# Kernel optimization log

Measured on AMD Instinct MI355X. Metric: run time of the kernel, lower is better.

The kernel has to match this reference:

```python
import jax, jax.numpy as jnp
import numpy as np

T, D, E, I = 2048, 2048, 16, 1408  # tokens, hidden, experts, moe intermediate


def setup_inputs() -> dict:
    key = jax.random.key(0)
    k1, k2, k3, k4 = jax.random.split(key, 4)
    return {
        "hidden_states": jax.random.normal(k1, (T, D), dtype=jnp.float32),
        "gate_w": jax.random.normal(k2, (E, D), dtype=jnp.float32) * 0.02,
        "w13": jax.random.normal(k3, (E, 2 * I, D), dtype=jnp.float32) * 0.02,
        "w2": jax.random.normal(k4, (E, D, I), dtype=jnp.float32) * 0.02,
        "top_k": 6,
    }


def reference(hidden_states, gate_w, w13, w2, top_k):
    x = hidden_states                               # [T, D]
    n_tokens, n_experts = x.shape[0], gate_w.shape[0]

    # Router gate + softmax + top-k (select_experts, use_grouped_topk=False)
    router_logits = x @ gate_w.T                    # [T, E]
    probs = jax.nn.softmax(router_logits, axis=-1)
    topk_w, topk_ids = jax.lax.top_k(probs, top_k)  # [T, K]
    # renormalize=True
    topk_w = topk_w / jnp.sum(topk_w, axis=-1, keepdims=True)

    # Dense combine weights [T, E]: scatter top-k weights to their experts
    combine = jnp.zeros((n_tokens, n_experts), dtype=x.dtype)
    combine = combine.at[jnp.arange(n_tokens)[:, None], topk_ids].add(topk_w)

    # Fused MoE experts: SwiGLU (w13 = fused gate+up), activation='silu'
    w1g = w13[:, : w13.shape[1] // 2, :]            # [E, I, D] gate proj
    w1u = w13[:, w13.shape[1] // 2 :, :]            # [E, I, D] up proj
    g = jnp.einsum("td,eid->tei", x, w1g)           # [T, E, I]
    u = jnp.einsum("td,eid->tei", x, w1u)
    h = jax.nn.silu(g) * u                          # [T, E, I]
    # Down proj + weighted combine over experts
    out = jnp.einsum("tei,edi,te->td", h, w2, combine)  # [T, D]
    return out
```

## Files before the change

### kernel.cpp

```cpp
#include <hip/hip_runtime.h>

#define T_TOK 2048
#define DIM 2048
#define NE 16
#define NI 1408
#define TOPK 6

typedef __bf16 bf16x8 __attribute__((ext_vector_type(8)));
typedef float f32x4 __attribute__((ext_vector_type(4)));

static __device__ __forceinline__ unsigned short f2bf(float f) {
  unsigned int u = __builtin_bit_cast(unsigned int, f);
  u += 0x7fffu + ((u >> 16) & 1u);
  return (unsigned short)(u >> 16);
}

static __device__ __forceinline__ void async_load16(const void* g, void* l) {
  __builtin_amdgcn_global_load_lds(
      (const __attribute__((address_space(1))) unsigned int*)g,
      (__attribute__((address_space(3))) unsigned int*)l, 16, 0, 0);
}

__global__ __launch_bounds__(256) void cvt_w_kernel(const float* __restrict__ w,
                                                    unsigned short* __restrict__ wb) {
  size_t i = ((size_t)blockIdx.x * 256 + threadIdx.x) * 8;
  float4 v0 = *(const float4*)(w + i);
  float4 v1 = *(const float4*)(w + i + 4);
  ushort4 o0 = make_ushort4(f2bf(v0.x), f2bf(v0.y), f2bf(v0.z), f2bf(v0.w));
  ushort4 o1 = make_ushort4(f2bf(v1.x), f2bf(v1.y), f2bf(v1.z), f2bf(v1.w));
  *(ushort4*)(wb + i) = o0;
  *(ushort4*)(wb + i + 4) = o1;
}

__global__ void router_kernel(const float* __restrict__ x, const float* __restrict__ gw,
                              float* __restrict__ combine) {
  int t = blockIdx.x;
  int l = threadIdx.x;
  const float* xr = x + (size_t)t * DIM;
  float acc[NE];
#pragma unroll
  for (int e = 0; e < NE; e++) acc[e] = 0.f;
  for (int d = l; d < DIM; d += 64) {
    float xv = xr[d];
#pragma unroll
    for (int e = 0; e < NE; e++) acc[e] += xv * gw[e * DIM + d];
  }
#pragma unroll
  for (int e = 0; e < NE; e++) {
    float v = acc[e];
#pragma unroll
    for (int s = 32; s > 0; s >>= 1) v += __shfl_down(v, s, 64);
    acc[e] = v;
  }
  if (l == 0) {
    float mx = acc[0];
#pragma unroll
    for (int e = 1; e < NE; e++) mx = fmaxf(mx, acc[e]);
    float p[NE]; float sum = 0.f;
#pragma unroll
    for (int e = 0; e < NE; e++) { p[e] = expf(acc[e] - mx); sum += p[e]; }
    float inv = 1.f / sum;
#pragma unroll
    for (int e = 0; e < NE; e++) p[e] *= inv;
    float w[NE];
#pragma unroll
    for (int e = 0; e < NE; e++) w[e] = 0.f;
    int used = 0;
    float ssum = 0.f;
    for (int k = 0; k < TOPK; k++) {
      int best = 0; float bv = -1e30f;
      for (int e = 0; e < NE; e++) {
        if (!((used >> e) & 1) && acc[e] > bv) { bv = acc[e]; best = e; }
      }
      used |= (1 << best);
      w[best] = p[best];
      ssum += p[best];
    }
    float isum = 1.f / ssum;
    for (int e = 0; e < NE; e++) combine[t * NE + e] = w[e] * isum;
  }
}

__global__ void cast_x_kernel(const float* __restrict__ x, unsigned short* __restrict__ xb) {
  int i = (blockIdx.x * 256 + threadIdx.x) * 4;
  float4 v = *(const float4*)(x + i);
  ushort4 o = make_ushort4(f2bf(v.x), f2bf(v.y), f2bf(v.z), f2bf(v.w));
  *(ushort4*)(xb + i) = o;
}

__global__ void count_kernel(const float* __restrict__ combine, int* __restrict__ counts) {
  int e = blockIdx.x, l = threadIdx.x;
  int c = 0;
  for (int t0 = 0; t0 < T_TOK; t0 += 64) {
    bool pred = combine[(size_t)(t0 + l) * NE + e] > 0.f;
    unsigned long long m = __ballot(pred);
    c += (int)__popcll(m);
  }
  if (l == 0) counts[e] = c;
}

__global__ void scan_kernel(const int* __restrict__ counts, int* __restrict__ offsets) {
  if (threadIdx.x == 0) {
    int s = 0;
    for (int e = 0; e < NE; e++) { offsets[e] = s; s += counts[e]; }
    offsets[NE] = s;
  }
}

__global__ void fill_kernel(const float* __restrict__ combine, const int* __restrict__ offsets,
                            int* __restrict__ ids, float* __restrict__ scales) {
  int e = blockIdx.x, l = threadIdx.x;
  int base = offsets[e];
  for (int t0 = 0; t0 < T_TOK; t0 += 64) {
    int t = t0 + l;
    float w = combine[(size_t)t * NE + e];
    bool pred = w > 0.f;
    unsigned long long m = __ballot(pred);
    int idx = base + (int)__popcll(m & ((1ull << l) - 1ull));
    if (pred) { ids[idx] = t; scales[idx] = w; }
    base += (int)__popcll(m);
  }
}

template<bool WBF16>
__global__ __launch_bounds__(256) void gemm1_kernel(
    const unsigned short* __restrict__ xb, const float* __restrict__ w13f,
    const unsigned short* __restrict__ w13b,
    const int* __restrict__ ids, const int* __restrict__ offsets,
    unsigned short* __restrict__ h) {
  int e = blockIdx.z;
  int off = offsets[e];
  int ne = offsets[e + 1] - off;
  int m0 = blockIdx.y * 128;
  if (m0 >= ne) return;
  int i0 = blockIdx.x * 64;

  __shared__ unsigned short At[8 * 128 * 8];
  __shared__ unsigned short Bg[8 * 64 * 8];
  __shared__ unsigned short Bu[8 * 64 * 8];
  __shared__ int ids_l[128];

  int tid = threadIdx.x;
  int wave = tid >> 6, lane = tid & 63;

  if (tid < 128) {
    int s = m0 + tid;
    ids_l[tid] = (s < ne) ? ids[off + s] : 0;
  }
  __syncthreads();
  int gid0 = ids_l[lane];
  int gid1 = ids_l[64 + lane];
  const unsigned short* a0 = xb + (size_t)gid0 * DIM;
  const unsigned short* a1 = xb + (size_t)gid1 * DIM;

  const float* Wg = nullptr; const float* Wu = nullptr;
  const unsigned short* WgB = nullptr; const unsigned short* WuB = nullptr;
  if constexpr (WBF16) {
    WgB = w13b + (size_t)e * (2 * NI) * DIM + (size_t)(i0 + lane) * DIM;
    WuB = WgB + (size_t)NI * DIM;
  } else {
    Wg = w13f + (size_t)e * (2 * NI) * DIM + (size_t)i0 * DIM;
    Wu = Wg + (size_t)NI * DIM;
  }

  int wm = wave >> 1, wn = wave & 1;
  int quad = lane >> 4, l15 = lane & 15;

  f32x4 zf = {0.f, 0.f, 0.f, 0.f};
  f32x4 accg[4][2], accu[4][2];
#pragma unroll
  for (int a = 0; a < 4; a++)
#pragma unroll
    for (int b = 0; b < 2; b++) { accg[a][b] = zf; accu[a][b] = zf; }

  int brow = tid >> 4;
  int c4 = tid & 15;
  int bchunk = c4 >> 1;
  int hof = (c4 & 1) * 4;

  for (int k0 = 0; k0 < DIM; k0 += 64) {
#pragma unroll
    for (int j = 0; j < 4; j++) {
      int linear = wave * 4 + j;
      int chunk = linear >> 1;
      int half = j & 1;
      const unsigned short* src = (half ? a1 : a0) + k0 + chunk * 8;
      async_load16(src, &At[chunk * 1024 + half * 512]);
    }
    if constexpr (WBF16) {
#pragma unroll
      for (int j = 0; j < 2; j++) {
        int chunk = wave * 2 + j;
        async_load16(WgB + k0 + chunk * 8, &Bg[chunk * 512]);
        async_load16(WuB + k0 + chunk * 8, &Bu[chunk * 512]);
      }
    } else {
#pragma unroll
      for (int r = 0; r < 4; r++) {
        int row = brow + r * 16;
        float4 vg = *(const float4*)(Wg + (size_t)row * DIM + k0 + c4 * 4);
        float4 vu = *(const float4*)(Wu + (size_t)row * DIM + k0 + c4 * 4);
        ushort4 og = make_ushort4(f2bf(vg.x), f2bf(vg.y), f2bf(vg.z), f2bf(vg.w));
        ushort4 ou = make_ushort4(f2bf(vu.x), f2bf(vu.y), f2bf(vu.z), f2bf(vu.w));
        *(ushort4*)&Bg[bchunk * 512 + row * 8 + hof] = og;
        *(ushort4*)&Bu[bchunk * 512 + row * 8 + hof] = ou;
      }
    }
    __syncthreads();
#pragma unroll
    for (int ks = 0; ks < 2; ks++) {
      int cb = ks * 4 + quad;
      bf16x8 af[4], bgf[2], buf_[2];
#pragma unroll
      for (int mt = 0; mt < 4; mt++)
        af[mt] = *(const bf16x8*)&At[cb * 1024 + (wm * 64 + mt * 16 + l15) * 8];
#pragma unroll
      for (int nt = 0; nt < 2; nt++) {
        bgf[nt] = *(const bf16x8*)&Bg[cb * 512 + (wn * 32 + nt * 16 + l15) * 8];
        buf_[nt] = *(const bf16x8*)&Bu[cb * 512 + (wn * 32 + nt * 16 + l15) * 8];
      }
#pragma unroll
      for (int mt = 0; mt < 4; mt++)
#pragma unroll
        for (int nt = 0; nt < 2; nt++) {
          accg[mt][nt] = __builtin_amdgcn_mfma_f32_16x16x32_bf16(af[mt], bgf[nt], accg[mt][nt], 0, 0, 0);
          accu[mt][nt] = __builtin_amdgcn_mfma_f32_16x16x32_bf16(af[mt], buf_[nt], accu[mt][nt], 0, 0, 0);
        }
    }
    __syncthreads();
  }
#pragma unroll
  for (int mt = 0; mt < 4; mt++)
#pragma unroll
    for (int nt = 0; nt < 2; nt++)
#pragma unroll
      for (int r = 0; r < 4; r++) {
        int row_l = wm * 64 + mt * 16 + quad * 4 + r;
        if (m0 + row_l < ne) {
          float gv = accg[mt][nt][r];
          float uv = accu[mt][nt][r];
          float hv = gv * uv / (1.f + __expf(-gv));
          int col = i0 + wn * 32 + nt * 16 + l15;
          h[(size_t)(off + m0 + row_l) * NI + col] = f2bf(hv);
        }
      }
}

template<bool WBF16>
__global__ __launch_bounds__(256) void gemm2_kernel(
    const unsigned short* __restrict__ h, const float* __restrict__ w2f,
    const unsigned short* __restrict__ w2b,
    const int* __restrict__ ids, const float* __restrict__ scales,
    const int* __restrict__ offsets, float* __restrict__ out) {
  int e = blockIdx.z;
  int off = offsets[e];
  int ne = offsets[e + 1] - off;
  int m0 = blockIdx.y * 128;
  if (m0 >= ne) return;
  int n0 = blockIdx.x * 128;

  __shared__ unsigned short At[8 * 128 * 8];
  __shared__ unsigned short Bt[8 * 128 * 8];
  __shared__ int ids_l[128];
  __shared__ float scl_l[128];

  int tid = threadIdx.x;
  int wave = tid >> 6, lane = tid & 63;
  if (tid < 128) {
    int s = m0 + tid;
    bool v = s < ne;
    ids_l[tid] = v ? ids[off + s] : 0;
    scl_l[tid] = v ? scales[off + s] : 0.f;
  }
  __syncthreads();

  const unsigned short* h0 = h + (size_t)(off + m0 + lane) * NI;
  const unsigned short* h1 = h + (size_t)(off + m0 + 64 + lane) * NI;

  const float* W = nullptr;
  const unsigned short* WB0 = nullptr; const unsigned short* WB1 = nullptr;
  if constexpr (WBF16) {
    WB0 = w2b + (size_t)e * DIM * NI + (size_t)(n0 + lane) * NI;
    WB1 = WB0 + (size_t)64 * NI;
  } else {
    W = w2f + (size_t)e * DIM * NI;
  }

  int wm = wave >> 1, wn = wave & 1;
  int quad = lane >> 4, l15 = lane & 15;

  f32x4 zf = {0.f, 0.f, 0.f, 0.f};
  f32x4 acc[4][4];
#pragma unroll
  for (int a = 0; a < 4; a++)
#pragma unroll
    for (int b = 0; b < 4; b++) acc[a][b] = zf;

  int brow = tid >> 4, c4 = tid & 15, bchunk = c4 >> 1, hof = (c4 & 1) * 4;

  for (int k0 = 0; k0 < NI; k0 += 64) {
#pragma unroll
    for (int j = 0; j < 4; j++) {
      int linear = wave * 4 + j;
      int chunk = linear >> 1;
      int half = j & 1;
      const unsigned short* src = (half ? h1 : h0) + k0 + chunk * 8;
      async_load16(src, &At[chunk * 1024 + half * 512]);
    }
    if constexpr (WBF16) {
#pragma unroll
      for (int j = 0; j < 4; j++) {
        int linear = wave * 4 + j;
        int chunk = linear >> 1;
        int half = j & 1;
        async_load16((half ? WB1 : WB0) + k0 + chunk * 8, &Bt[chunk * 1024 + half * 512]);
      }
    } else {
#pragma unroll
      for (int r = 0; r < 8; r++) {
        int row = brow + r * 16;
        float4 v = *(const float4*)(W + (size_t)(n0 + row) * NI + k0 + c4 * 4);
        ushort4 o = make_ushort4(f2bf(v.x), f2bf(v.y), f2bf(v.z), f2bf(v.w));
        *(ushort4*)&Bt[bchunk * 1024 + row * 8 + hof] = o;
      }
    }
    __syncthreads();
#pragma unroll
    for (int ks = 0; ks < 2; ks++) {
      int cb = ks * 4 + quad;
      bf16x8 af[4], bf[4];
#pragma unroll
      for (int mt = 0; mt < 4; mt++)
        af[mt] = *(const bf16x8*)&At[cb * 1024 + (wm * 64 + mt * 16 + l15) * 8];
#pragma unroll
      for (int nt = 0; nt < 4; nt++)
        bf[nt] = *(const bf16x8*)&Bt[cb * 1024 + (wn * 64 + nt * 16 + l15) * 8];
#pragma unroll
      for (int mt = 0; mt < 4; mt++)
#pragma unroll
        for (int nt = 0; nt < 4; nt++)
          acc[mt][nt] = __builtin_amdgcn_mfma_f32_16x16x32_bf16(af[mt], bf[nt], acc[mt][nt], 0, 0, 0);
    }
    __syncthreads();
  }
#pragma unroll
  for (int mt = 0; mt < 4; mt++)
#pragma unroll
    for (int nt = 0; nt < 4; nt++)
#pragma unroll
      for (int r = 0; r < 4; r++) {
        int row_l = wm * 64 + mt * 16 + quad * 4 + r;
        if (m0 + row_l < ne) {
          int t = ids_l[row_l];
          float s = scl_l[row_l];
          int col = n0 + wn * 64 + nt * 16 + l15;
          atomicAdd(&out[(size_t)t * DIM + col], s * acc[mt][nt][r]);
        }
      }
}

extern "C" void kernel_launch(void* const* d_in, const int* in_sizes, int n_in,
                              void* d_out, int out_size, void* d_ws, size_t ws_size,
                              hipStream_t stream) {
  const float* x   = (const float*)d_in[0];
  const float* gw  = (const float*)d_in[1];
  const float* w13 = (const float*)d_in[2];
  const float* w2  = (const float*)d_in[3];
  float* out = (float*)d_out;

  char* ws = (char*)d_ws;
  float* combine        = (float*)(ws + 0x000000);
  int* counts           = (int*)  (ws + 0x020000);
  int* offsets          = (int*)  (ws + 0x020100);
  int* ids              = (int*)  (ws + 0x020200);
  float* scales         = (float*)(ws + 0x02D000);
  unsigned short* xb    = (unsigned short*)(ws + 0x040000);
  unsigned short* h     = (unsigned short*)(ws + 0x840000);

  const size_t n13 = (size_t)NE * 2 * NI * DIM;
  const size_t n2  = (size_t)NE * DIM * NI;
  size_t hend = 0x840000 + (size_t)(12288 + 128) * NI * 2;
  size_t w13off = (hend + 255) & ~(size_t)255;
  size_t w2off  = w13off + n13 * 2;
  size_t need13   = w2off;
  size_t needfull = w2off + n2 * 2;
  bool b13 = ws_size >= need13;
  bool b2  = ws_size >= needfull;
  unsigned short* w13b = (unsigned short*)(ws + w13off);
  unsigned short* w2b  = (unsigned short*)(ws + w2off);

  hipMemsetAsync(d_out, 0, (size_t)T_TOK * DIM * sizeof(float), stream);

  if (b13) cvt_w_kernel<<<(int)(n13 / (256 * 8)), 256, 0, stream>>>(w13, w13b);
  if (b2)  cvt_w_kernel<<<(int)(n2  / (256 * 8)), 256, 0, stream>>>(w2, w2b);

  router_kernel<<<T_TOK, 64, 0, stream>>>(x, gw, combine);
  cast_x_kernel<<<(T_TOK * DIM) / (256 * 4), 256, 0, stream>>>(x, xb);
  count_kernel<<<NE, 64, 0, stream>>>(combine, counts);
  scan_kernel<<<1, 64, 0, stream>>>(counts, offsets);
  fill_kernel<<<NE, 64, 0, stream>>>(combine, offsets, ids, scales);

  if (b13)
    gemm1_kernel<true><<<dim3(NI / 64, T_TOK / 128, NE), 256, 0, stream>>>(xb, nullptr, w13b, ids, offsets, h);
  else
    gemm1_kernel<false><<<dim3(NI / 64, T_TOK / 128, NE), 256, 0, stream>>>(xb, w13, nullptr, ids, offsets, h);

  if (b2)
    gemm2_kernel<true><<<dim3(DIM / 128, T_TOK / 128, NE), 256, 0, stream>>>(h, nullptr, w2b, ids, scales, offsets, out);
  else
    gemm2_kernel<false><<<dim3(DIM / 128, T_TOK / 128, NE), 256, 0, stream>>>(h, w2, nullptr, ids, scales, offsets, out);
}
```

Before: 1.233 ms.

## Register-prefetch next K tile in both expert GEMMs instead of async LDS loads

Both grouped GEMM kernels (gate/up and down projection) stop using direct global-to-LDS async loads. They now load the next K tile into registers while the MFMAs of the current tile run, then write it to LDS after a barrier. The loads become contiguous 16-byte per-row reads, and the fp32 weight path converts to bf16 in registers during staging. This hides global memory latency behind compute, at the cost of higher register pressure and an extra LDS write pass per tile.

Result: no change. 1.230 ms (-0.2%).

```diff
diff --git a/kernel.cpp b/kernel.cpp
--- a/kernel.cpp
+++ b/kernel.cpp
@@ -8,6 +8,7 @@
 
 typedef __bf16 bf16x8 __attribute__((ext_vector_type(8)));
 typedef float f32x4 __attribute__((ext_vector_type(4)));
+typedef unsigned short u16x8 __attribute__((ext_vector_type(8)));
 
 static __device__ __forceinline__ unsigned short f2bf(float f) {
   unsigned int u = __builtin_bit_cast(unsigned int, f);
@@ -15,10 +16,11 @@
   return (unsigned short)(u >> 16);
 }
 
-static __device__ __forceinline__ void async_load16(const void* g, void* l) {
-  __builtin_amdgcn_global_load_lds(
-      (const __attribute__((address_space(1))) unsigned int*)g,
-      (__attribute__((address_space(3))) unsigned int*)l, 16, 0, 0);
+static __device__ __forceinline__ u16x8 cvt8(float4 a, float4 b) {
+  u16x8 r;
+  r[0] = f2bf(a.x); r[1] = f2bf(a.y); r[2] = f2bf(a.z); r[3] = f2bf(a.w);
+  r[4] = f2bf(b.x); r[5] = f2bf(b.y); r[6] = f2bf(b.z); r[7] = f2bf(b.w);
+  return r;
 }
 
 __global__ __launch_bounds__(256) void cvt_w_kernel(const float* __restrict__ w,
@@ -26,10 +28,7 @@
   size_t i = ((size_t)blockIdx.x * 256 + threadIdx.x) * 8;
   float4 v0 = *(const float4*)(w + i);
   float4 v1 = *(const float4*)(w + i + 4);
-  ushort4 o0 = make_ushort4(f2bf(v0.x), f2bf(v0.y), f2bf(v0.z), f2bf(v0.w));
-  ushort4 o1 = make_ushort4(f2bf(v1.x), f2bf(v1.y), f2bf(v1.z), f2bf(v1.w));
-  *(ushort4*)(wb + i) = o0;
-  *(ushort4*)(wb + i + 4) = o1;
+  *(u16x8*)(wb + i) = cvt8(v0, v1);
 }
 
 __global__ void router_kernel(const float* __restrict__ x, const float* __restrict__ gw,
@@ -148,20 +147,58 @@
     ids_l[tid] = (s < ne) ? ids[off + s] : 0;
   }
   __syncthreads();
-  int gid0 = ids_l[lane];
-  int gid1 = ids_l[64 + lane];
-  const unsigned short* a0 = xb + (size_t)gid0 * DIM;
-  const unsigned short* a1 = xb + (size_t)gid1 * DIM;
-
-  const float* Wg = nullptr; const float* Wu = nullptr;
-  const unsigned short* WgB = nullptr; const unsigned short* WuB = nullptr;
+
+  int ra = tid & 127, ca0 = tid >> 7;
+  const unsigned short* arow = xb + (size_t)ids_l[ra] * DIM;
+  int rb = tid & 63, cb0 = tid >> 6;
+  const unsigned short* growB = nullptr; const unsigned short* urowB = nullptr;
+  const float* growF = nullptr; const float* urowF = nullptr;
   if constexpr (WBF16) {
-    WgB = w13b + (size_t)e * (2 * NI) * DIM + (size_t)(i0 + lane) * DIM;
-    WuB = WgB + (size_t)NI * DIM;
+    growB = w13b + ((size_t)e * 2 * NI + i0 + rb) * DIM;
+    urowB = growB + (size_t)NI * DIM;
   } else {
-    Wg = w13f + (size_t)e * (2 * NI) * DIM + (size_t)i0 * DIM;
-    Wu = Wg + (size_t)NI * DIM;
-  }
+    growF = w13f + ((size_t)e * 2 * NI + i0 + rb) * DIM;
+    urowF = growF + (size_t)NI * DIM;
+  }
+
+  u16x8 pa[4], pbg[2], pbu[2];
+  float4 fbg[2][2], fbu[2][2];
+
+  auto loadA = [&](int k0) {
+#pragma unroll
+    for (int j = 0; j < 4; j++) pa[j] = *(const u16x8*)(arow + k0 + (ca0 + 2 * j) * 8);
+  };
+  auto loadB = [&](int k0) {
+    if constexpr (WBF16) {
+#pragma unroll
+      for (int j = 0; j < 2; j++) {
+        pbg[j] = *(const u16x8*)(growB + k0 + (cb0 + 4 * j) * 8);
+        pbu[j] = *(const u16x8*)(urowB + k0 + (cb0 + 4 * j) * 8);
+      }
+    } else {
+#pragma unroll
+      for (int j = 0; j < 2; j++) {
+        const float* g = growF + k0 + (cb0 + 4 * j) * 8;
+        const float* u = urowF + k0 + (cb0 + 4 * j) * 8;
+        fbg[j][0] = *(const float4*)g; fbg[j][1] = *(const float4*)(g + 4);
+        fbu[j][0] = *(const float4*)u; fbu[j][1] = *(const float4*)(u + 4);
+      }
+    }
+  };
+  auto stage = [&]() {
+#pragma unroll
+    for (int j = 0; j < 4; j++) *(u16x8*)&At[(ca0 + 2 * j) * 1024 + ra * 8] = pa[j];
+#pragma unroll
+    for (int j = 0; j < 2; j++) {
+      if constexpr (WBF16) {
+        *(u16x8*)&Bg[(cb0 + 4 * j) * 512 + rb * 8] = pbg[j];
+        *(u16x8*)&Bu[(cb0 + 4 * j) * 512 + rb * 8] = pbu[j];
+      } else {
+        *(u16x8*)&Bg[(cb0 + 4 * j) * 512 + rb * 8] = cvt8(fbg[j][0], fbg[j][1]);
+        *(u16x8*)&Bu[(cb0 + 4 * j) * 512 + rb * 8] = cvt8(fbu[j][0], fbu[j][1]);
+      }
+    }
+  };
 
   int wm = wave >> 1, wn = wave & 1;
   int quad = lane >> 4, l15 = lane & 15;
@@ -173,40 +210,12 @@
 #pragma unroll
     for (int b = 0; b < 2; b++) { accg[a][b] = zf; accu[a][b] = zf; }
 
-  int brow = tid >> 4;
-  int c4 = tid & 15;
-  int bchunk = c4 >> 1;
-  int hof = (c4 & 1) * 4;
-
+  loadA(0); loadB(0);
   for (int k0 = 0; k0 < DIM; k0 += 64) {
-#pragma unroll
-    for (int j = 0; j < 4; j++) {
-      int linear = wave * 4 + j;
-      int chunk = linear >> 1;
-      int half = j & 1;
-      const unsigned short* src = (half ? a1 : a0) + k0 + chunk * 8;
-      async_load16(src, &At[chunk * 1024 + half * 512]);
-    }
-    if constexpr (WBF16) {
-#pragma unroll
-      for (int j = 0; j < 2; j++) {
-        int chunk = wave * 2 + j;
-        async_load16(WgB + k0 + chunk * 8, &Bg[chunk * 512]);
-        async_load16(WuB + k0 + chunk * 8, &Bu[chunk * 512]);
-      }
-    } else {
-#pragma unroll
-      for (int r = 0; r < 4; r++) {
-        int row = brow + r * 16;
-        float4 vg = *(const float4*)(Wg + (size_t)row * DIM + k0 + c4 * 4);
-        float4 vu = *(const float4*)(Wu + (size_t)row * DIM + k0 + c4 * 4);
-        ushort4 og = make_ushort4(f2bf(vg.x), f2bf(vg.y), f2bf(vg.z), f2bf(vg.w));
-        ushort4 ou = make_ushort4(f2bf(vu.x), f2bf(vu.y), f2bf(vu.z), f2bf(vu.w));
-        *(ushort4*)&Bg[bchunk * 512 + row * 8 + hof] = og;
-        *(ushort4*)&Bu[bchunk * 512 + row * 8 + hof] = ou;
-      }
-    }
     __syncthreads();
+    stage();
+    __syncthreads();
+    if (k0 + 64 < DIM) { loadA(k0 + 64); loadB(k0 + 64); }
 #pragma unroll
     for (int ks = 0; ks < 2; ks++) {
       int cb = ks * 4 + quad;
@@ -227,7 +236,6 @@
           accu[mt][nt] = __builtin_amdgcn_mfma_f32_16x16x32_bf16(af[mt], buf_[nt], accu[mt][nt], 0, 0, 0);
         }
     }
-    __syncthreads();
   }
 #pragma unroll
   for (int mt = 0; mt < 4; mt++)
@@ -274,17 +282,42 @@
   }
   __syncthreads();
 
-  const unsigned short* h0 = h + (size_t)(off + m0 + lane) * NI;
-  const unsigned short* h1 = h + (size_t)(off + m0 + 64 + lane) * NI;
-
-  const float* W = nullptr;
-  const unsigned short* WB0 = nullptr; const unsigned short* WB1 = nullptr;
-  if constexpr (WBF16) {
-    WB0 = w2b + (size_t)e * DIM * NI + (size_t)(n0 + lane) * NI;
-    WB1 = WB0 + (size_t)64 * NI;
-  } else {
-    W = w2f + (size_t)e * DIM * NI;
-  }
+  int ra = tid & 127, ca0 = tid >> 7;
+  const unsigned short* arow = h + (size_t)(off + m0 + ra) * NI;
+  int rb = tid & 127, cb0 = tid >> 7;
+  const unsigned short* browB = nullptr;
+  const float* browF = nullptr;
+  if constexpr (WBF16) browB = w2b + ((size_t)e * DIM + n0 + rb) * NI;
+  else                 browF = w2f + ((size_t)e * DIM + n0 + rb) * NI;
+
+  u16x8 pa[4], pb[4];
+  float4 fb[4][2];
+
+  auto loadA = [&](int k0) {
+#pragma unroll
+    for (int j = 0; j < 4; j++) pa[j] = *(const u16x8*)(arow + k0 + (ca0 + 2 * j) * 8);
+  };
+  auto loadB = [&](int k0) {
+    if constexpr (WBF16) {
+#pragma unroll
+      for (int j = 0; j < 4; j++) pb[j] = *(const u16x8*)(browB + k0 + (cb0 + 2 * j) * 8);
+    } else {
+#pragma unroll
+      for (int j = 0; j < 4; j++) {
+        const float* g = browF + k0 + (cb0 + 2 * j) * 8;
+        fb[j][0] = *(const float4*)g; fb[j][1] = *(const float4*)(g + 4);
+      }
+    }
+  };
+  auto stage = [&]() {
+#pragma unroll
+    for (int j = 0; j < 4; j++) *(u16x8*)&At[(ca0 + 2 * j) * 1024 + ra * 8] = pa[j];
+#pragma unroll
+    for (int j = 0; j < 4; j++) {
+      if constexpr (WBF16) *(u16x8*)&Bt[(cb0 + 2 * j) * 1024 + rb * 8] = pb[j];
+      else                 *(u16x8*)&Bt[(cb0 + 2 * j) * 1024 + rb * 8] = cvt8(fb[j][0], fb[j][1]);
+    }
+  };
 
   int wm = wave >> 1, wn = wave & 1;
   int quad = lane >> 4, l15 = lane & 15;
@@ -296,35 +329,12 @@
 #pragma unroll
     for (int b = 0; b < 4; b++) acc[a][b] = zf;
 
-  int brow = tid >> 4, c4 = tid & 15, bchunk = c4 >> 1, hof = (c4 & 1) * 4;
-
+  loadA(0); loadB(0);
   for (int k0 = 0; k0 < NI; k0 += 64) {
-#pragma unroll
-    for (int j = 0; j < 4; j++) {
-      int linear = wave * 4 + j;
-      int chunk = linear >> 1;
-      int half = j & 1;
-      const unsigned short* src = (half ? h1 : h0) + k0 + chunk * 8;
-      async_load16(src, &At[chunk * 1024 + half * 512]);
-    }
-    if constexpr (WBF16) {
-#pragma unroll
-      for (int j = 0; j < 4; j++) {
-        int linear = wave * 4 + j;
-        int chunk = linear >> 1;
-        int half = j & 1;
-        async_load16((half ? WB1 : WB0) + k0 + chunk * 8, &Bt[chunk * 1024 + half * 512]);
-      }
-    } else {
-#pragma unroll
-      for (int r = 0; r < 8; r++) {
-        int row = brow + r * 16;
-        float4 v = *(const float4*)(W + (size_t)(n0 + row) * NI + k0 + c4 * 4);
-        ushort4 o = make_ushort4(f2bf(v.x), f2bf(v.y), f2bf(v.z), f2bf(v.w));
-        *(ushort4*)&Bt[bchunk * 1024 + row * 8 + hof] = o;
-      }
-    }
     __syncthreads();
+    stage();
+    __syncthreads();
+    if (k0 + 64 < NI) { loadA(k0 + 64); loadB(k0 + 64); }
 #pragma unroll
     for (int ks = 0; ks < 2; ks++) {
       int cb = ks * 4 + quad;
@@ -341,7 +351,6 @@
         for (int nt = 0; nt < 4; nt++)
           acc[mt][nt] = __builtin_amdgcn_mfma_f32_16x16x32_bf16(af[mt], bf[nt], acc[mt][nt], 0, 0, 0);
     }
-    __syncthreads();
   }
 #pragma unroll
   for (int mt = 0; mt < 4; mt++)
```
